# Optimization experiments

Hardware: AMD Instinct MI355X
Metric: run time of the kernel (lower is better)

Reference implementation:

```python
import jax, jax.numpy as jnp
import numpy as np

B, L, D, H, NE, M = 4, 1024, 768, 12, 42, 8
OFFSET = 1
NEG = -1e9

def setup_inputs() -> dict:
    key = jax.random.key(0)
    k1, k2, k3, k4 = jax.random.split(key, 4)
    sequence_output = jax.random.normal(k1, (B, L, D), dtype=jnp.float32)
    attention = jax.random.uniform(k2, (B, H, L, L), dtype=jnp.float32)
    mention_idx = jax.random.randint(k3, (B, NE, M), 0, L - 2).astype(jnp.int32)
    mention_mask = jax.random.randint(k4, (B, NE, M), 0, 2).astype(jnp.int32)
    mention_mask = mention_mask.at[:, :, 0].set(1)  # every entity has >=1 mention
    return {"sequence_output": sequence_output, "attention": attention,
            "mention_idx": mention_idx, "mention_mask": mention_mask}

def reference(sequence_output, attention, mention_idx, mention_mask):
    b, l, d = sequence_output.shape
    h = attention.shape[1]
    idx = mention_idx + OFFSET                      # start + offset
    valid = (mention_mask > 0) & (idx < l)          # [B,NE,M], mirrors start+offset < c check
    idx = jnp.where(valid, idx, 0)

    # --- get_hrt: entity embedding = logsumexp over mentions, entity attn = mean over mentions ---
    flat = idx.reshape(b, -1)
    emb = jax.vmap(lambda s, i: s[i])(sequence_output, flat).reshape(b, NE, M, d)
    masked = jnp.where(valid[..., None], emb, NEG)
    ent_emb = jax.nn.logsumexp(masked, axis=2)      # [B,NE,D] (unused downstream, kept faithful)

    att = jax.vmap(lambda a, i: a[:, i])(attention, flat)        # [B,H,NE*M,L]
    att = att.reshape(b, h, NE, M, l)
    vmask = valid.astype(att.dtype)[:, None, :, :, None]         # [B,1,NE,M,1]
    cnt = jnp.maximum(valid.sum(axis=2), 1).astype(att.dtype)    # [B,NE]
    ent_att = (att * vmask).sum(axis=3) / cnt[:, None, :, None]  # [B,H,NE,L]

    # --- get_channel_map: ht_att = mean_h(h_att * t_att), row-normalize, contract with tokens ---
    ht_att = jnp.einsum('bhsl,bhtl->bstl', ent_att, ent_att) / h  # [B,NE,NE,L]
    ht_att = ht_att / (ht_att.sum(axis=-1, keepdims=True) + 1e-5)
    feature_map = jnp.einsum('bstl,bld->bstd', ht_att, sequence_output)  # [B,NE,NE,D]
    return feature_map
```

## Files before the change

kernel.cpp:

```cpp
#include <hip/hip_runtime.h>

#define B_    4
#define L_    1024
#define D_    768
#define H_    12
#define NE_   42
#define M_    8
#define NE2_  (NE_ * NE_)
#define MPAD_ 1792

typedef unsigned short u16;
typedef unsigned int   u32;

__device__ __forceinline__ u16 f2bf(float f) {
    union { float f; u32 u; } c; c.f = f;
    u32 u = c.u;
    u32 r = (u + 0x7FFFu + ((u >> 16) & 1u)) >> 16;
    return (u16)r;
}

__global__ __launch_bounds__(128) void ent_att_kernel(
    const float* __restrict__ att, const int* __restrict__ midx,
    const int* __restrict__ mmask, float* __restrict__ ent) {
    const int h = blockIdx.x, e = blockIdx.y, b = blockIdx.z;
    const int t  = threadIdx.x;
    const int l0 = t * 8;
    const int mb = (b * NE_ + e) * M_;
    const size_t abase = ((size_t)(b * H_ + h)) * L_ * L_;

    float acc[8] = {0.f,0.f,0.f,0.f,0.f,0.f,0.f,0.f};
    int cnt = 0;
    for (int m = 0; m < M_; ++m) {
        int  im = midx[mb + m] + 1;
        bool v  = (mmask[mb + m] > 0) && (im < L_);
        if (v) {
            ++cnt;
            const float* row = att + abase + (size_t)im * L_ + l0;
            float4 x0 = *(const float4*)(row);
            float4 x1 = *(const float4*)(row + 4);
            acc[0] += x0.x; acc[1] += x0.y; acc[2] += x0.z; acc[3] += x0.w;
            acc[4] += x1.x; acc[5] += x1.y; acc[6] += x1.z; acc[7] += x1.w;
        }
    }
    const float s = 1.0f / (float)(cnt < 1 ? 1 : cnt);
    float* o = ent + (((size_t)(b * H_ + h)) * NE_ + e) * L_ + l0;
    *(float4*)(o)     = make_float4(acc[0]*s, acc[1]*s, acc[2]*s, acc[3]*s);
    *(float4*)(o + 4) = make_float4(acc[4]*s, acc[5]*s, acc[6]*s, acc[7]*s);
}

__global__ __launch_bounds__(256) void transpose_kernel(
    const float* __restrict__ S, u16* __restrict__ T) {
    __shared__ u16 tile[32][33];
    const int b  = blockIdx.z;
    const int n0 = blockIdx.x * 32;
    const int k0 = blockIdx.y * 32;
    const int tx = threadIdx.x, ty = threadIdx.y;
    const float* Sb = S + (size_t)b * L_ * D_;
    u16*         Tb = T + (size_t)b * D_ * L_;
    #pragma unroll
    for (int i = 0; i < 4; ++i)
        tile[ty + i*8][tx] = f2bf(Sb[(size_t)(k0 + ty + i*8) * D_ + (n0 + tx)]);
    __syncthreads();
    #pragma unroll
    for (int i = 0; i < 4; ++i)
        Tb[(size_t)(n0 + ty + i*8) * L_ + (k0 + tx)] = tile[tx][ty + i*8];
}

__global__ __launch_bounds__(128) void w_kernel(
    const float* __restrict__ ent, u16* __restrict__ W) {
    const int p = blockIdx.x % MPAD_;
    const int b = blockIdx.x / MPAD_;
    const int t  = threadIdx.x;
    const int l0 = t * 8;
    u16* wrow = W + ((size_t)b * MPAD_ + p) * L_;

    if (p >= NE2_) {
        uint4 z; z.x = z.y = z.z = z.w = 0u;
        *(uint4*)(wrow + l0) = z;
        return;
    }
    const int s  = p / NE_;
    const int tt = p % NE_;
    const float* Eb = ent + (size_t)b * H_ * NE_ * L_;

    float acc[8] = {0.f,0.f,0.f,0.f,0.f,0.f,0.f,0.f};
    for (int h = 0; h < H_; ++h) {
        const float4* as = (const float4*)(Eb + ((size_t)(h * NE_ + s))  * L_ + l0);
        const float4* at = (const float4*)(Eb + ((size_t)(h * NE_ + tt)) * L_ + l0);
        float4 a0 = as[0], a1 = as[1], b0 = at[0], b1 = at[1];
        acc[0] += a0.x * b0.x; acc[1] += a0.y * b0.y;
        acc[2] += a0.z * b0.z; acc[3] += a0.w * b0.w;
        acc[4] += a1.x * b1.x; acc[5] += a1.y * b1.y;
        acc[6] += a1.z * b1.z; acc[7] += a1.w * b1.w;
    }
    float local = acc[0]+acc[1]+acc[2]+acc[3]+acc[4]+acc[5]+acc[6]+acc[7];
    #pragma unroll
    for (int off = 32; off > 0; off >>= 1) local += __shfl_xor(local, off, 64);
    __shared__ float red[2];
    const int wv = t >> 6, ln = t & 63;
    if (ln == 0) red[wv] = local;
    __syncthreads();
    const float tot = red[0] + red[1];
    const float inv = 1.0f / (tot + (float)H_ * 1e-5f);

    u32 w0 = (u32)f2bf(acc[0]*inv) | ((u32)f2bf(acc[1]*inv) << 16);
    u32 w1 = (u32)f2bf(acc[2]*inv) | ((u32)f2bf(acc[3]*inv) << 16);
    u32 w2 = (u32)f2bf(acc[4]*inv) | ((u32)f2bf(acc[5]*inv) << 16);
    u32 w3 = (u32)f2bf(acc[6]*inv) | ((u32)f2bf(acc[7]*inv) << 16);
    uint4 o; o.x = w0; o.y = w1; o.z = w2; o.w = w3;
    *(uint4*)(wrow + l0) = o;
}

typedef __attribute__((ext_vector_type(8))) __bf16 bf16x8;
typedef __attribute__((ext_vector_type(4))) float  f32x4;

__global__ __launch_bounds__(256) void gemm_kernel(
    const u16* __restrict__ W, const u16* __restrict__ T, float* __restrict__ out) {
    __shared__ __align__(16) u16 As[128 * 32];
    __shared__ __align__(16) u16 Bs[128 * 32];
    const int b = blockIdx.z;
    const u16* Ab = W + (size_t)b * MPAD_ * L_ + (size_t)blockIdx.x * 128 * L_;
    const u16* Bb = T + (size_t)b * D_   * L_ + (size_t)blockIdx.y * 128 * L_;
    const int tid  = threadIdx.x;
    const int wave = tid >> 6, lane = tid & 63;
    const int wm = (wave & 1) * 64, wn = (wave >> 1) * 64;
    const int rm = lane & 15, kq = (lane >> 4) * 8;

    f32x4 acc[4][4] = {};

    for (int k0 = 0; k0 < L_; k0 += 32) {
        __syncthreads();
        #pragma unroll
        for (int i = 0; i < 2; ++i) {
            int c = i * 256 + tid;
            int row = c >> 2, ko = (c & 3) * 8;
            __builtin_amdgcn_global_load_lds(
                (const __attribute__((address_space(1))) void*)(Ab + (size_t)row * L_ + k0 + ko),
                (__attribute__((address_space(3))) void*)(&As[c * 8]), 16, 0, 0);
            __builtin_amdgcn_global_load_lds(
                (const __attribute__((address_space(1))) void*)(Bb + (size_t)row * L_ + k0 + ko),
                (__attribute__((address_space(3))) void*)(&Bs[c * 8]), 16, 0, 0);
        }
        __syncthreads();

        bf16x8 af[4], bfr[4];
        #pragma unroll
        for (int i = 0; i < 4; ++i)
            af[i]  = *(const bf16x8*)&As[(wm + i*16 + rm) * 32 + kq];
        #pragma unroll
        for (int j = 0; j < 4; ++j)
            bfr[j] = *(const bf16x8*)&Bs[(wn + j*16 + rm) * 32 + kq];
        #pragma unroll
        for (int i = 0; i < 4; ++i)
            #pragma unroll
            for (int j = 0; j < 4; ++j)
                acc[i][j] = __builtin_amdgcn_mfma_f32_16x16x32_bf16(
                                af[i], bfr[j], acc[i][j], 0, 0, 0);
    }

    const int row0 = blockIdx.x * 128 + wm;
    const int col0 = blockIdx.y * 128 + wn;
    const int cl = lane & 15, rq = (lane >> 4) * 4;
    float* Ob = out + (size_t)b * NE2_ * D_;
    #pragma unroll
    for (int i = 0; i < 4; ++i) {
        #pragma unroll
        for (int j = 0; j < 4; ++j) {
            const int col = col0 + j*16 + cl;
            #pragma unroll
            for (int r = 0; r < 4; ++r) {
                const int row = row0 + i*16 + rq + r;
                if (row < NE2_)
                    Ob[(size_t)row * D_ + col] = acc[i][j][r];
            }
        }
    }
}

#define ENT_BYTES (8257536)
#define W_BYTES   (14680064)

extern "C" void kernel_launch(void* const* d_in, const int* in_sizes, int n_in,
                              void* d_out, int out_size, void* d_ws, size_t ws_size,
                              hipStream_t stream) {
    const float* seq   = (const float*)d_in[0];
    const float* att   = (const float*)d_in[1];
    const int*   midx  = (const int*)d_in[2];
    const int*   mmask = (const int*)d_in[3];
    float* out = (float*)d_out;

    char* ws  = (char*)d_ws;
    float* ent = (float*)ws;
    u16*   W   = (u16*)(ws + ENT_BYTES);
    u16*   ST  = (u16*)(ws + ENT_BYTES + W_BYTES);

    ent_att_kernel<<<dim3(H_, NE_, B_), 128, 0, stream>>>(att, midx, mmask, ent);
    transpose_kernel<<<dim3(D_/32, L_/32, B_), dim3(32, 8), 0, stream>>>(seq, ST);
    w_kernel<<<B_ * MPAD_, 128, 0, stream>>>(ent, W);
    gemm_kernel<<<dim3(MPAD_/128, D_/128, B_), 256, 0, stream>>>(W, ST, out);
}
```

Measured before the change: 315.9 us.

## Exploit symmetry of ht_att: compute upper-triangle pairs only and mirror outputs

Because the entity-pair attention product is symmetric in (s,t), the W matrix now covers only the 903 upper-triangle pairs, padded to 1024 rows instead of 1792. The GEMM M dimension roughly halves, and the epilogue writes each result row to both (s,t) and (t,s). The per-pair work is replaced by a gram kernel that stages L-chunks of ent in shared memory and computes 2x4 register tiles. Row normalisation is deferred: per-chunk partial sums feed a small rscale kernel, and the GEMM epilogue applies the scale. This adds an extra launch, a sqrt-based triangular index decode, and duplicated output stores.

```diff
diff --git a/kernel.cpp b/kernel.cpp
--- a/kernel.cpp
+++ b/kernel.cpp
@@ -1,4 +1,5 @@
 #include <hip/hip_runtime.h>
+#include <math.h>
 
 #define B_    4
 #define L_    1024
@@ -7,10 +8,14 @@
 #define NE_   42
 #define M_    8
 #define NE2_  (NE_ * NE_)
-#define MPAD_ 1792
+#define NTRI_ 903
+#define MPAD_ 1024
+#define LC_   16
+#define NCH_  (L_ / LC_)
 
 typedef unsigned short u16;
 typedef unsigned int   u32;
+typedef __attribute__((ext_vector_type(2))) float f32x2;
 
 __device__ __forceinline__ u16 f2bf(float f) {
     union { float f; u32 u; } c; c.f = f;
@@ -66,56 +71,107 @@
         Tb[(size_t)(n0 + ty + i*8) * L_ + (k0 + tx)] = tile[tx][ty + i*8];
 }
 
-__global__ __launch_bounds__(128) void w_kernel(
-    const float* __restrict__ ent, u16* __restrict__ W) {
-    const int p = blockIdx.x % MPAD_;
-    const int b = blockIdx.x / MPAD_;
-    const int t  = threadIdx.x;
-    const int l0 = t * 8;
-    u16* wrow = W + ((size_t)b * MPAD_ + p) * L_;
-
-    if (p >= NE2_) {
-        uint4 z; z.x = z.y = z.z = z.w = 0u;
-        *(uint4*)(wrow + l0) = z;
-        return;
-    }
-    const int s  = p / NE_;
-    const int tt = p % NE_;
-    const float* Eb = ent + (size_t)b * H_ * NE_ * L_;
-
-    float acc[8] = {0.f,0.f,0.f,0.f,0.f,0.f,0.f,0.f};
-    for (int h = 0; h < H_; ++h) {
-        const float4* as = (const float4*)(Eb + ((size_t)(h * NE_ + s))  * L_ + l0);
-        const float4* at = (const float4*)(Eb + ((size_t)(h * NE_ + tt)) * L_ + l0);
-        float4 a0 = as[0], a1 = as[1], b0 = at[0], b1 = at[1];
-        acc[0] += a0.x * b0.x; acc[1] += a0.y * b0.y;
-        acc[2] += a0.z * b0.z; acc[3] += a0.w * b0.w;
-        acc[4] += a1.x * b1.x; acc[5] += a1.y * b1.y;
-        acc[6] += a1.z * b1.z; acc[7] += a1.w * b1.w;
-    }
-    float local = acc[0]+acc[1]+acc[2]+acc[3]+acc[4]+acc[5]+acc[6]+acc[7];
-    #pragma unroll
-    for (int off = 32; off > 0; off >>= 1) local += __shfl_xor(local, off, 64);
-    __shared__ float red[2];
-    const int wv = t >> 6, ln = t & 63;
-    if (ln == 0) red[wv] = local;
+__global__ __launch_bounds__(256) void gram_kernel(
+    const float* __restrict__ ent,
+    u16* __restrict__ W,
+    float* __restrict__ psum)
+{
+    __shared__ float E[H_ * NE_ * 18 + 8];
+    const int gid   = blockIdx.x;
+    const int xcd   = gid & 7, rr = gid >> 3;
+    const int chunk = xcd * 8 + (rr & 7);
+    const int b     = rr >> 3;
+    const int l0    = chunk * LC_;
+    const int tid   = threadIdx.x;
+
+    const float* Eb = ent + (size_t)b * (H_ * NE_) * L_ + l0;
+    for (int i = tid; i < H_ * NE_ * 4; i += 256) {
+        const int row = i >> 2, sub = (i & 3) * 4;
+        float4 v = *(const float4*)(Eb + (size_t)row * L_ + sub);
+        f32x2* d = (f32x2*)&E[row * 18 + sub];
+        d[0] = f32x2{v.x, v.y};
+        d[1] = f32x2{v.z, v.w};
+    }
     __syncthreads();
-    const float tot = red[0] + red[1];
-    const float inv = 1.0f / (tot + (float)H_ * 1e-5f);
-
-    u32 w0 = (u32)f2bf(acc[0]*inv) | ((u32)f2bf(acc[1]*inv) << 16);
-    u32 w1 = (u32)f2bf(acc[2]*inv) | ((u32)f2bf(acc[3]*inv) << 16);
-    u32 w2 = (u32)f2bf(acc[4]*inv) | ((u32)f2bf(acc[5]*inv) << 16);
-    u32 w3 = (u32)f2bf(acc[6]*inv) | ((u32)f2bf(acc[7]*inv) << 16);
-    uint4 o; o.x = w0; o.y = w1; o.z = w2; o.w = w3;
-    *(uint4*)(wrow + l0) = o;
+
+    if (tid < 231) {
+        const int st = tid % 21, tt = tid / 21;
+        const int s0 = 2 * st, t0 = 4 * tt;
+        if (s0 <= t0 + 3) {
+            const int e2 = (t0 + 2 < NE_) ? t0 + 2 : NE_ - 1;
+            const int e3 = (t0 + 3 < NE_) ? t0 + 3 : NE_ - 1;
+            float ps[2][4] = {};
+            for (int l2 = 0; l2 < LC_ / 2; ++l2) {
+                const int ll = 2 * l2;
+                f32x2 c[2][4] = {};
+                #pragma unroll
+                for (int h = 0; h < H_; ++h) {
+                    const float* Eh = E + h * (NE_ * 18);
+                    f32x2 a0 = *(const f32x2*)&Eh[(s0    ) * 18 + ll];
+                    f32x2 a1 = *(const f32x2*)&Eh[(s0 + 1) * 18 + ll];
+                    f32x2 b0 = *(const f32x2*)&Eh[(t0    ) * 18 + ll];
+                    f32x2 b1 = *(const f32x2*)&Eh[(t0 + 1) * 18 + ll];
+                    f32x2 b2 = *(const f32x2*)&Eh[(e2    ) * 18 + ll];
+                    f32x2 b3 = *(const f32x2*)&Eh[(e3    ) * 18 + ll];
+                    c[0][0] += a0 * b0; c[0][1] += a0 * b1;
+                    c[0][2] += a0 * b2; c[0][3] += a0 * b3;
+                    c[1][0] += a1 * b0; c[1][1] += a1 * b1;
+                    c[1][2] += a1 * b2; c[1][3] += a1 * b3;
+                }
+                #pragma unroll
+                for (int si = 0; si < 2; ++si) {
+                    #pragma unroll
+                    for (int tj = 0; tj < 4; ++tj) {
+                        const int s = s0 + si, t = t0 + tj;
+                        if (t < NE_ && s <= t) {
+                            const int q = (s * (85 - s)) / 2 + (t - s);
+                            u32 w = (u32)f2bf(c[si][tj][0]) |
+                                    ((u32)f2bf(c[si][tj][1]) << 16);
+                            *(u32*)(W + ((size_t)b * MPAD_ + q) * L_ + l0 + ll) = w;
+                            ps[si][tj] += c[si][tj][0] + c[si][tj][1];
+                        }
+                    }
+                }
+            }
+            #pragma unroll
+            for (int si = 0; si < 2; ++si)
+                #pragma unroll
+                for (int tj = 0; tj < 4; ++tj) {
+                    const int s = s0 + si, t = t0 + tj;
+                    if (t < NE_ && s <= t) {
+                        const int q = (s * (85 - s)) / 2 + (t - s);
+                        psum[((size_t)b * MPAD_ + q) * NCH_ + chunk] = ps[si][tj];
+                    }
+                }
+        }
+    } else {
+        for (int q = NTRI_ + (tid - 231); q < MPAD_; q += 25) {
+            u16* wr = W + ((size_t)b * MPAD_ + q) * L_ + l0;
+            uint4 z; z.x = z.y = z.z = z.w = 0u;
+            *(uint4*)(wr)     = z;
+            *(uint4*)(wr + 8) = z;
+        }
+    }
+}
+
+__global__ __launch_bounds__(256) void rscale_kernel(
+    const float* __restrict__ psum, float* __restrict__ rscale) {
+    const int g = blockIdx.x * 256 + threadIdx.x;
+    if (g >= B_ * NTRI_) return;
+    const int b = g / NTRI_, q = g % NTRI_;
+    const float* p = psum + ((size_t)b * MPAD_ + q) * NCH_;
+    float s = 0.f;
+    #pragma unroll
+    for (int i = 0; i < NCH_; ++i) s += p[i];
+    rscale[b * MPAD_ + q] = 1.0f / (s + (float)H_ * 1e-5f);
 }
 
 typedef __attribute__((ext_vector_type(8))) __bf16 bf16x8;
 typedef __attribute__((ext_vector_type(4))) float  f32x4;
 
 __global__ __launch_bounds__(256) void gemm_kernel(
-    const u16* __restrict__ W, const u16* __restrict__ T, float* __restrict__ out) {
+    const u16* __restrict__ W, const u16* __restrict__ T,
+    const float* __restrict__ rscale, float* __restrict__ out) {
     __shared__ __align__(16) u16 As[128 * 32];
     __shared__ __align__(16) u16 Bs[128 * 32];
     const int b = blockIdx.z;
@@ -162,23 +218,38 @@
     const int col0 = blockIdx.y * 128 + wn;
     const int cl = lane & 15, rq = (lane >> 4) * 4;
     float* Ob = out + (size_t)b * NE2_ * D_;
+    const float* rsb = rscale + (size_t)b * MPAD_;
     #pragma unroll
     for (int i = 0; i < 4; ++i) {
         #pragma unroll
-        for (int j = 0; j < 4; ++j) {
-            const int col = col0 + j*16 + cl;
-            #pragma unroll
-            for (int r = 0; r < 4; ++r) {
-                const int row = row0 + i*16 + rq + r;
-                if (row < NE2_)
-                    Ob[(size_t)row * D_ + col] = acc[i][j][r];
+        for (int r = 0; r < 4; ++r) {
+            const int q = row0 + i*16 + rq + r;
+            if (q < NTRI_) {
+                int s = (int)(42.5f - sqrtf(1806.25f - 2.0f * (float)q));
+                if (s < 0) s = 0; if (s > 41) s = 41;
+                int base = (s * (85 - s)) >> 1;
+                if (q < base) { --s; base = (s * (85 - s)) >> 1; }
+                else { const int nb = ((s + 1) * (84 - s)) >> 1;
+                       if (q >= nb) { ++s; base = nb; } }
+                const int t = s + (q - base);
+                const float sc = rsb[q];
+                float* O1 = Ob + (size_t)(s * NE_ + t) * D_ + col0 + cl;
+                float* O2 = Ob + (size_t)(t * NE_ + s) * D_ + col0 + cl;
+                #pragma unroll
+                for (int j = 0; j < 4; ++j) {
+                    const float v = acc[i][j][r] * sc;
+                    O1[j * 16] = v;
+                    O2[j * 16] = v;
+                }
             }
         }
     }
 }
 
-#define ENT_BYTES (8257536)
-#define W_BYTES   (14680064)
+#define ENT_BYTES  (8257536)
+#define W_BYTES    (8388608)
+#define ST_BYTES   (6291456)
+#define PSUM_BYTES (1048576)
 
 extern "C" void kernel_launch(void* const* d_in, const int* in_sizes, int n_in,
                               void* d_out, int out_size, void* d_ws, size_t ws_size,
@@ -190,12 +261,15 @@
     float* out = (float*)d_out;
 
     char* ws  = (char*)d_ws;
-    float* ent = (float*)ws;
-    u16*   W   = (u16*)(ws + ENT_BYTES);
-    u16*   ST  = (u16*)(ws + ENT_BYTES + W_BYTES);
+    float* ent    = (float*)ws;
+    u16*   W      = (u16*)(ws + ENT_BYTES);
+    u16*   ST     = (u16*)(ws + ENT_BYTES + W_BYTES);
+    float* psum   = (float*)(ws + ENT_BYTES + W_BYTES + ST_BYTES);
+    float* rscale = (float*)(ws + ENT_BYTES + W_BYTES + ST_BYTES + PSUM_BYTES);
 
     ent_att_kernel<<<dim3(H_, NE_, B_), 128, 0, stream>>>(att, midx, mmask, ent);
     transpose_kernel<<<dim3(D_/32, L_/32, B_), dim3(32, 8), 0, stream>>>(seq, ST);
-    w_kernel<<<B_ * MPAD_, 128, 0, stream>>>(ent, W);
-    gemm_kernel<<<dim3(MPAD_/128, D_/128, B_), 256, 0, stream>>>(W, ST, out);
-}
+    gram_kernel<<<256, 256, 0, stream>>>(ent, W, psum);
+    rscale_kernel<<<(B_ * NTRI_ + 255) / 256, 256, 0, stream>>>(psum, rscale);
+    gemm_kernel<<<dim3(MPAD_/128, D_/128, B_), 256, 0, stream>>>(W, ST, rscale, out);
+}
```

Result: faster. 299.3 us (-5.3%).
